# Kernel optimization log

Hardware: AMD Instinct MI355X
Metric: run time of the kernel (lower is better)

The kernel has to match this reference:

```python
import jax, jax.numpy as jnp
import numpy as np

INV2 = 0.5  # (1/sqrt(2))^2 for separable 2D haar


def haar_dwt2(x):
    """Single-level 2D haar DWT, pywt convention (symmetric mode, even dims).
    x: (B, H, W) -> cA, cH, cV, cD each (B, H/2, W/2).
    pywt keys: cA='aa', cH='ad' (approx rows, detail cols), cV='da', cD='dd';
    1D haar: a=(x0+x1)/sqrt2, d=(x0-x1)/sqrt2.
    """
    B, H, W = x.shape
    b = x.reshape(B, H // 2, 2, W // 2, 2)
    x00 = b[:, :, 0, :, 0]
    x01 = b[:, :, 0, :, 1]
    x10 = b[:, :, 1, :, 0]
    x11 = b[:, :, 1, :, 1]
    cA = (x00 + x01 + x10 + x11) * INV2
    cH = (x00 - x01 + x10 - x11) * INV2
    cV = (x00 + x01 - x10 - x11) * INV2
    cD = (x00 - x01 - x10 + x11) * INV2
    return cA, cH, cV, cD


def bilinear_up(x, H, W):
    """Half-pixel bilinear resize (== torch align_corners=False). x: (B,h,w)."""
    return jax.image.resize(x, (x.shape[0], H, W), method='bilinear')


def setup_inputs() -> dict:
    key = jax.random.key(0)
    x = jax.random.normal(key, (32, 1, 1024, 1024), dtype=jnp.float32)
    return {"x": x}


def reference(x):
    B, _, H, W = x.shape
    img = x[:, 0]  # (B, H, W)
    # level 1
    cA1, cH1, cV1, cD1 = haar_dwt2(img)            # (B, H/2, W/2)
    # level 2 on approximation
    cA2, cH2, cV2, cD2 = haar_dwt2(cA1)            # (B, H/4, W/4)
    h1, w1 = cH1.shape[1], cH1.shape[2]
    cH2u = bilinear_up(cH2, h1, w1)
    cV2u = bilinear_up(cV2, h1, w1)
    cD2u = bilinear_up(cD2, h1, w1)
    # (B, 6, H/2, W/2)
    return jnp.stack([cH1, cV1, cD1, cH2u, cV2u, cD2u], axis=1)
```

## Files before the change

kernel.cpp:

```cpp
#include <hip/hip_runtime.h>


#define HW_IN 1024
#define HW_L1 512
#define HW_L2 256

template <bool WRITE_A>
__global__ __launch_bounds__(256) void dwt_l1_kernel(const float* __restrict__ x,
                                                     float* __restrict__ out,
                                                     float* __restrict__ cA)
{
    int idx = blockIdx.x * blockDim.x + threadIdx.x;
    int jj = idx & 255;
    int t  = idx >> 8;
    int i  = t & 511;
    int b  = t >> 9;

    const float* xb = x + ((size_t)b << 20);
    const float4 r0 = ((const float4*)(xb + ((size_t)(2 * i)     << 10)))[jj];
    const float4 r1 = ((const float4*)(xb + ((size_t)(2 * i + 1) << 10)))[jj];

    float a0 = (r0.x + r0.y + r1.x + r1.y) * 0.5f;
    float h0 = (r0.x - r0.y + r1.x - r1.y) * 0.5f;
    float v0 = (r0.x + r0.y - r1.x - r1.y) * 0.5f;
    float d0 = (r0.x - r0.y - r1.x + r1.y) * 0.5f;
    float a1 = (r0.z + r0.w + r1.z + r1.w) * 0.5f;
    float h1 = (r0.z - r0.w + r1.z - r1.w) * 0.5f;
    float v1 = (r0.z + r0.w - r1.z - r1.w) * 0.5f;
    float d1 = (r0.z - r0.w - r1.z + r1.w) * 0.5f;

    const size_t plane  = (size_t)HW_L1 * HW_L1;
    const size_t rowoff = (size_t)i * HW_L1 + 2 * jj;
    float* ob = out + (size_t)b * 6 * plane;
    *(float2*)(ob + 0 * plane + rowoff) = make_float2(h0, h1);
    *(float2*)(ob + 1 * plane + rowoff) = make_float2(v0, v1);
    *(float2*)(ob + 2 * plane + rowoff) = make_float2(d0, d1);
    if (WRITE_A)
        *(float2*)(cA + (size_t)b * plane + rowoff) = make_float2(a0, a1);
}

template <bool USE_WS>
__global__ __launch_bounds__(256) void dwt_l2_up_kernel(const float* __restrict__ x,
                                                        const float* __restrict__ cA,
                                                        float* __restrict__ out)
{
    int j = blockIdx.x * 16 + threadIdx.x;
    int i = blockIdx.y * 16 + threadIdx.y;
    int b = blockIdx.z;

    int   p0 = (i - 1) >> 1;
    int   p1 = p0 + 1;
    float fi = (i & 1) ? 0.25f : 0.75f;
    int   q0 = (j - 1) >> 1;
    int   q1 = q0 + 1;
    float fj = (j & 1) ? 0.25f : 0.75f;
    p0 = max(p0, 0); p1 = min(p1, HW_L2 - 1);
    q0 = max(q0, 0); q1 = min(q1, HW_L2 - 1);

    auto getA = [&](int r, int c) -> float {
        if (USE_WS)
            return cA[((size_t)b << 18) + ((size_t)r << 9) + c];
        const float* xb = x + ((size_t)b << 20) + ((size_t)(2 * r) << 10) + 2 * c;
        return (xb[0] + xb[1] + xb[HW_IN] + xb[HW_IN + 1]) * 0.5f;
    };

    float h[2][2], v[2][2], d[2][2];
    int ps[2] = {p0, p1}, qs[2] = {q0, q1};
#pragma unroll
    for (int pi = 0; pi < 2; ++pi) {
#pragma unroll
        for (int qi = 0; qi < 2; ++qi) {
            int p = ps[pi], q = qs[qi];
            float a00 = getA(2 * p,     2 * q);
            float a01 = getA(2 * p,     2 * q + 1);
            float a10 = getA(2 * p + 1, 2 * q);
            float a11 = getA(2 * p + 1, 2 * q + 1);
            h[pi][qi] = (a00 - a01 + a10 - a11) * 0.5f;
            v[pi][qi] = (a00 + a01 - a10 - a11) * 0.5f;
            d[pi][qi] = (a00 - a01 - a10 + a11) * 0.5f;
        }
    }

    float w00 = (1.f - fi) * (1.f - fj), w01 = (1.f - fi) * fj;
    float w10 = fi * (1.f - fj),         w11 = fi * fj;

    float H = w00 * h[0][0] + w01 * h[0][1] + w10 * h[1][0] + w11 * h[1][1];
    float V = w00 * v[0][0] + w01 * v[0][1] + w10 * v[1][0] + w11 * v[1][1];
    float D = w00 * d[0][0] + w01 * d[0][1] + w10 * d[1][0] + w11 * d[1][1];

    const size_t plane = (size_t)HW_L1 * HW_L1;
    float* ob = out + (size_t)b * 6 * plane + (size_t)i * HW_L1 + j;
    ob[3 * plane] = H;
    ob[4 * plane] = V;
    ob[5 * plane] = D;
}

extern "C" void kernel_launch(void* const* d_in, const int* in_sizes, int n_in,
                              void* d_out, int out_size, void* d_ws, size_t ws_size,
                              hipStream_t stream)
{
    const float* x = (const float*)d_in[0];
    float* out = (float*)d_out;
    float* cA  = (float*)d_ws;

    int B = in_sizes[0] >> 20;
    size_t ws_needed = (size_t)B * HW_L1 * HW_L1 * sizeof(float);
    bool use_ws = (ws_size >= ws_needed);

    int n1 = B * HW_L1 * (HW_L1 / 2);
    dim3 grid2((HW_L1 + 15) / 16, (HW_L1 + 15) / 16, B);
    dim3 block2(16, 16, 1);

    if (use_ws) {
        dwt_l1_kernel<true><<<n1 / 256, 256, 0, stream>>>(x, out, cA);
        dwt_l2_up_kernel<true><<<grid2, block2, 0, stream>>>(x, cA, out);
    } else {
        dwt_l1_kernel<false><<<n1 / 256, 256, 0, stream>>>(x, out, nullptr);
        dwt_l2_up_kernel<false><<<grid2, block2, 0, stream>>>(x, nullptr, out);
    }
}
```

Baseline: 322.0 us.

## Fuse both DWT levels and upsampling into one LDS-tiled kernel

New measurement: 312.0 us. 1.03x faster.

```diff
diff --git a/kernel.cpp b/kernel.cpp
--- a/kernel.cpp
+++ b/kernel.cpp
@@ -1,98 +1,123 @@
 #include <hip/hip_runtime.h>
 
 
-#define HW_IN 1024
 #define HW_L1 512
-#define HW_L2 256
+#define PLANE ((size_t)HW_L1 * HW_L1)
+#define TILE 64
+#define LH 68
+#define LW 70
 
-template <bool WRITE_A>
-__global__ __launch_bounds__(256) void dwt_l1_kernel(const float* __restrict__ x,
-                                                     float* __restrict__ out,
-                                                     float* __restrict__ cA)
+__global__ __launch_bounds__(256) void dwt_fused_kernel(const float* __restrict__ x,
+                                                        float* __restrict__ out)
 {
-    int idx = blockIdx.x * blockDim.x + threadIdx.x;
-    int jj = idx & 255;
-    int t  = idx >> 8;
-    int i  = t & 511;
-    int b  = t >> 9;
+    __shared__ float lds[LH * LW];
+
+    const int tid = threadIdx.x;
+    const int b  = blockIdx.z;
+    const int i0 = blockIdx.y * TILE;
+    const int j0 = blockIdx.x * TILE;
 
     const float* xb = x + ((size_t)b << 20);
-    const float4 r0 = ((const float4*)(xb + ((size_t)(2 * i)     << 10)))[jj];
-    const float4 r1 = ((const float4*)(xb + ((size_t)(2 * i + 1) << 10)))[jj];
+    float* ob = out + (size_t)b * 6 * PLANE;
 
-    float a0 = (r0.x + r0.y + r1.x + r1.y) * 0.5f;
-    float h0 = (r0.x - r0.y + r1.x - r1.y) * 0.5f;
-    float v0 = (r0.x + r0.y - r1.x - r1.y) * 0.5f;
-    float d0 = (r0.x - r0.y - r1.x + r1.y) * 0.5f;
-    float a1 = (r0.z + r0.w + r1.z + r1.w) * 0.5f;
-    float h1 = (r0.z - r0.w + r1.z - r1.w) * 0.5f;
-    float v1 = (r0.z + r0.w - r1.z - r1.w) * 0.5f;
-    float d1 = (r0.z - r0.w - r1.z + r1.w) * 0.5f;
+    {
+        const int tx = tid & 31;
+        const int ty = tid >> 5;
+        const int f4 = (j0 >> 1) + tx;
+#pragma unroll
+        for (int k = 0; k < 8; ++k) {
+            const int il = k * 8 + ty;
+            const int i  = i0 + il;
+            const float4 r0 = ((const float4*)(xb + ((size_t)(2 * i)     << 10)))[f4];
+            const float4 r1 = ((const float4*)(xb + ((size_t)(2 * i + 1) << 10)))[f4];
 
-    const size_t plane  = (size_t)HW_L1 * HW_L1;
-    const size_t rowoff = (size_t)i * HW_L1 + 2 * jj;
-    float* ob = out + (size_t)b * 6 * plane;
-    *(float2*)(ob + 0 * plane + rowoff) = make_float2(h0, h1);
-    *(float2*)(ob + 1 * plane + rowoff) = make_float2(v0, v1);
-    *(float2*)(ob + 2 * plane + rowoff) = make_float2(d0, d1);
-    if (WRITE_A)
-        *(float2*)(cA + (size_t)b * plane + rowoff) = make_float2(a0, a1);
-}
+            const float a0 = (r0.x + r0.y + r1.x + r1.y) * 0.5f;
+            const float h0 = (r0.x - r0.y + r1.x - r1.y) * 0.5f;
+            const float v0 = (r0.x + r0.y - r1.x - r1.y) * 0.5f;
+            const float d0 = (r0.x - r0.y - r1.x + r1.y) * 0.5f;
+            const float a1 = (r0.z + r0.w + r1.z + r1.w) * 0.5f;
+            const float h1 = (r0.z - r0.w + r1.z - r1.w) * 0.5f;
+            const float v1 = (r0.z + r0.w - r1.z - r1.w) * 0.5f;
+            const float d1 = (r0.z - r0.w - r1.z + r1.w) * 0.5f;
 
-template <bool USE_WS>
-__global__ __launch_bounds__(256) void dwt_l2_up_kernel(const float* __restrict__ x,
-                                                        const float* __restrict__ cA,
-                                                        float* __restrict__ out)
-{
-    int j = blockIdx.x * 16 + threadIdx.x;
-    int i = blockIdx.y * 16 + threadIdx.y;
-    int b = blockIdx.z;
-
-    int   p0 = (i - 1) >> 1;
-    int   p1 = p0 + 1;
-    float fi = (i & 1) ? 0.25f : 0.75f;
-    int   q0 = (j - 1) >> 1;
-    int   q1 = q0 + 1;
-    float fj = (j & 1) ? 0.25f : 0.75f;
-    p0 = max(p0, 0); p1 = min(p1, HW_L2 - 1);
-    q0 = max(q0, 0); q1 = min(q1, HW_L2 - 1);
-
-    auto getA = [&](int r, int c) -> float {
-        if (USE_WS)
-            return cA[((size_t)b << 18) + ((size_t)r << 9) + c];
-        const float* xb = x + ((size_t)b << 20) + ((size_t)(2 * r) << 10) + 2 * c;
-        return (xb[0] + xb[1] + xb[HW_IN] + xb[HW_IN + 1]) * 0.5f;
-    };
-
-    float h[2][2], v[2][2], d[2][2];
-    int ps[2] = {p0, p1}, qs[2] = {q0, q1};
-#pragma unroll
-    for (int pi = 0; pi < 2; ++pi) {
-#pragma unroll
-        for (int qi = 0; qi < 2; ++qi) {
-            int p = ps[pi], q = qs[qi];
-            float a00 = getA(2 * p,     2 * q);
-            float a01 = getA(2 * p,     2 * q + 1);
-            float a10 = getA(2 * p + 1, 2 * q);
-            float a11 = getA(2 * p + 1, 2 * q + 1);
-            h[pi][qi] = (a00 - a01 + a10 - a11) * 0.5f;
-            v[pi][qi] = (a00 + a01 - a10 - a11) * 0.5f;
-            d[pi][qi] = (a00 - a01 - a10 + a11) * 0.5f;
+            const size_t ro = (size_t)i * HW_L1 + j0 + 2 * tx;
+            *(float2*)(ob + 0 * PLANE + ro) = make_float2(h0, h1);
+            *(float2*)(ob + 1 * PLANE + ro) = make_float2(v0, v1);
+            *(float2*)(ob + 2 * PLANE + ro) = make_float2(d0, d1);
+            *(float2*)(&lds[(il + 2) * LW + 2 * tx + 2]) = make_float2(a0, a1);
         }
     }
 
-    float w00 = (1.f - fi) * (1.f - fj), w01 = (1.f - fi) * fj;
-    float w10 = fi * (1.f - fj),         w11 = fi * fj;
+    for (int c = tid; c < 528; c += 256) {
+        int lr, lc;
+        if (c < 136)      { lr = c / 68;                lc = c % 68; }
+        else if (c < 272) { lr = 66 + (c - 136) / 68;   lc = (c - 136) % 68; }
+        else { int s = c - 272; lr = 2 + (s >> 2); int m = s & 3; lc = (m < 2) ? m : 64 + m; }
+        const int gi = min(max(i0 + lr - 2, 0), HW_L1 - 1);
+        const int gj = min(max(j0 + lc - 2, 0), HW_L1 - 1);
+        const float* p = xb + ((size_t)(2 * gi) << 10) + 2 * gj;
+        lds[lr * LW + lc] = (p[0] + p[1] + p[1024] + p[1025]) * 0.5f;
+    }
 
-    float H = w00 * h[0][0] + w01 * h[0][1] + w10 * h[1][0] + w11 * h[1][1];
-    float V = w00 * v[0][0] + w01 * v[0][1] + w10 * v[1][0] + w11 * v[1][1];
-    float D = w00 * d[0][0] + w01 * d[0][1] + w10 * d[1][0] + w11 * d[1][1];
+    __syncthreads();
 
-    const size_t plane = (size_t)HW_L1 * HW_L1;
-    float* ob = out + (size_t)b * 6 * plane + (size_t)i * HW_L1 + j;
-    ob[3 * plane] = H;
-    ob[4 * plane] = V;
-    ob[5 * plane] = D;
+    {
+        const int jl = tid & 63;
+        const int j  = j0 + jl;
+        const int q0u = (j - 1) >> 1;
+        const int q1  = min(q0u + 1, 255);
+        const int q0  = max(q0u, 0);
+        const float fj = (j & 1) ? 0.25f : 0.75f;
+        const int c0 = 2 * q0 - j0 + 2;
+        const int c1 = 2 * q1 - j0 + 2;
+
+#pragma unroll
+        for (int k = 0; k < 16; ++k) {
+            const int il = k * 4 + (tid >> 6);
+            const int i  = i0 + il;
+            const int p0u = (i - 1) >> 1;
+            const int p1  = min(p0u + 1, 255);
+            const int p0  = max(p0u, 0);
+            const float fi = (i & 1) ? 0.25f : 0.75f;
+            const int ra = 2 * p0 - i0 + 2;
+            const int rb = 2 * p1 - i0 + 2;
+
+            const float2 t00 = *(const float2*)&lds[ra * LW + c0];
+            const float2 t01 = *(const float2*)&lds[ra * LW + c1];
+            const float2 t10 = *(const float2*)&lds[(ra + 1) * LW + c0];
+            const float2 t11 = *(const float2*)&lds[(ra + 1) * LW + c1];
+            const float2 u00 = *(const float2*)&lds[rb * LW + c0];
+            const float2 u01 = *(const float2*)&lds[rb * LW + c1];
+            const float2 u10 = *(const float2*)&lds[(rb + 1) * LW + c0];
+            const float2 u11 = *(const float2*)&lds[(rb + 1) * LW + c1];
+
+            const float sm_t0 = t00.x - t00.y, sp_t0 = t00.x + t00.y;
+            const float sm_b0 = t10.x - t10.y, sp_b0 = t10.x + t10.y;
+            const float sm_t1 = t01.x - t01.y, sp_t1 = t01.x + t01.y;
+            const float sm_b1 = t11.x - t11.y, sp_b1 = t11.x + t11.y;
+            const float sm_T0 = u00.x - u00.y, sp_T0 = u00.x + u00.y;
+            const float sm_B0 = u10.x - u10.y, sp_B0 = u10.x + u10.y;
+            const float sm_T1 = u01.x - u01.y, sp_T1 = u01.x + u01.y;
+            const float sm_B1 = u11.x - u11.y, sp_B1 = u11.x + u11.y;
+
+            const float h00 = (sm_t0 + sm_b0) * 0.5f, v00 = (sp_t0 - sp_b0) * 0.5f, d00 = (sm_t0 - sm_b0) * 0.5f;
+            const float h01 = (sm_t1 + sm_b1) * 0.5f, v01 = (sp_t1 - sp_b1) * 0.5f, d01 = (sm_t1 - sm_b1) * 0.5f;
+            const float h10 = (sm_T0 + sm_B0) * 0.5f, v10 = (sp_T0 - sp_B0) * 0.5f, d10 = (sm_T0 - sm_B0) * 0.5f;
+            const float h11 = (sm_T1 + sm_B1) * 0.5f, v11 = (sp_T1 - sp_B1) * 0.5f, d11 = (sm_T1 - sm_B1) * 0.5f;
+
+            const float w00 = (1.f - fi) * (1.f - fj), w01 = (1.f - fi) * fj;
+            const float w10 = fi * (1.f - fj),         w11 = fi * fj;
+
+            const float H = w00 * h00 + w01 * h01 + w10 * h10 + w11 * h11;
+            const float V = w00 * v00 + w01 * v01 + w10 * v10 + w11 * v11;
+            const float D = w00 * d00 + w01 * d01 + w10 * d10 + w11 * d11;
+
+            const size_t oo = (size_t)i * HW_L1 + j;
+            ob[3 * PLANE + oo] = H;
+            ob[4 * PLANE + oo] = V;
+            ob[5 * PLANE + oo] = D;
+        }
+    }
 }
 
 extern "C" void kernel_launch(void* const* d_in, const int* in_sizes, int n_in,
@@ -101,21 +126,8 @@
 {
     const float* x = (const float*)d_in[0];
     float* out = (float*)d_out;
-    float* cA  = (float*)d_ws;
+    const int B = in_sizes[0] >> 20;
 
-    int B = in_sizes[0] >> 20;
-    size_t ws_needed = (size_t)B * HW_L1 * HW_L1 * sizeof(float);
-    bool use_ws = (ws_size >= ws_needed);
-
-    int n1 = B * HW_L1 * (HW_L1 / 2);
-    dim3 grid2((HW_L1 + 15) / 16, (HW_L1 + 15) / 16, B);
-    dim3 block2(16, 16, 1);
-
-    if (use_ws) {
-        dwt_l1_kernel<true><<<n1 / 256, 256, 0, stream>>>(x, out, cA);
-        dwt_l2_up_kernel<true><<<grid2, block2, 0, stream>>>(x, cA, out);
-    } else {
-        dwt_l1_kernel<false><<<n1 / 256, 256, 0, stream>>>(x, out, nullptr);
-        dwt_l2_up_kernel<false><<<grid2, block2, 0, stream>>>(x, nullptr, out);
-    }
+    dim3 grid(HW_L1 / TILE, HW_L1 / TILE, B);
+    dwt_fused_kernel<<<grid, 256, 0, stream>>>(x, out);
 }
```
